# Optimization experiments

Measured on AMD Instinct MI355X. Metric: run time of the kernel, lower is better.

Reference implementation:

```python
import jax, jax.numpy as jnp
import numpy as np

NH = 16          # num_attention_heads
SMAX = 400.0     # smax for previous-task gates

def _gelu(x):
    return jax.nn.gelu(x, approximate=False)

def setup_inputs() -> dict:
    key = jax.random.key(0)
    ks = jax.random.split(key, 18)
    B, S, H, A, N = 8, 2048, 1024, 512, 10
    sc = lambda fan: 1.0 / np.sqrt(fan)
    f32 = jnp.float32
    return {
        "x":     jax.random.normal(ks[0], (B, S, H), f32),
        "fc1_w": jax.random.normal(ks[1], (A, H), f32) * sc(H),
        "fc1_b": jnp.zeros((A,), f32),
        "fc2_w": jax.random.normal(ks[2], (H, A), f32) * sc(A),
        "fc2_b": jnp.zeros((H,), f32),
        "efc1":  jax.random.normal(ks[3], (N, A), f32),
        "efc2":  jax.random.normal(ks[4], (N, H), f32),
        "etask": jax.random.normal(ks[5], (N, H), f32),
        "q_w":   jax.random.normal(ks[6], (H, H), f32) * sc(H),
        "q_b":   jnp.zeros((H,), f32),
        "k_w":   jax.random.normal(ks[7], (H, H), f32) * sc(H),
        "k_b":   jnp.zeros((H,), f32),
        "v_w":   jax.random.normal(ks[8], (H, H), f32) * sc(H),
        "v_b":   jnp.zeros((H,), f32),
        "equery": jax.random.normal(ks[9],  (N, H), f32),
        "ekey":   jax.random.normal(ks[10], (N, H), f32),
        "evalue": jax.random.normal(ks[11], (N, H), f32),
        "t": 5,
        "s": 400,
    }

def reference(x, fc1_w, fc1_b, fc2_w, fc2_b, efc1, efc2, etask,
              q_w, q_b, k_w, k_b, v_w, v_b, equery, ekey, evalue, t, s):
    B, S, H = x.shape
    hd = H // NH
    s = jnp.float32(s)

    # --- current-task gated adapter: h = act(fc2(act(fc1(x)) * gfc1)) * gfc2 ---
    h1 = _gelu(x @ fc1_w.T + fc1_b)                         # [B,S,A]
    gfc1 = jax.nn.sigmoid(s * efc1[t])                      # [A]
    gfc2 = jax.nn.sigmoid(s * efc2[t])                      # [H]
    h = _gelu((h1 * gfc1) @ fc2_w.T + fc2_b) * gfc2         # [B,S,H]

    # --- previous tasks (detached, gates at smax); vectorized over pre_t ---
    pg1 = jax.nn.sigmoid(SMAX * efc1[:t])                   # [t,A]
    pg2 = jax.nn.sigmoid(SMAX * efc2[:t])                   # [t,H]
    pre_h1 = h1[:, None, :, :] * pg1[None, :, None, :]      # [B,t,S,A]
    pre_h = _gelu(jnp.einsum('btsa,ha->btsh', pre_h1, fc2_w) + fc2_b)
    pre_h = jax.lax.stop_gradient(pre_h * pg2[None, :, None, :])  # [B,t,S,H]

    hid = jnp.concatenate([h[:, None], pre_h], axis=1)      # [B,T,S,H], T=t+1
    Tn = t + 1

    # --- task-gated QKV ---
    t_emb = jnp.broadcast_to(etask[t], (B, 1, S, H))        # query_states
    gq = jax.nn.sigmoid(s * equery[t])
    gk = jax.nn.sigmoid(s * ekey[t])
    gv = jax.nn.sigmoid(s * evalue[t])
    q = (t_emb @ q_w.T + q_b) * gq                          # [B,1,S,H]
    k = (hid @ k_w.T + k_b) * gk                            # [B,T,S,H]
    v = (hid @ v_w.T + v_b) * gv                            # [B,T,S,H]

    q5 = q.reshape(B, 1, S, NH, hd)
    k5 = k.reshape(B, Tn, S, NH, hd)
    v5 = v.reshape(B, Tn, S, NH, hd)

    # torch permute algebra: contract over heads (n), softmax over tasks (t)
    scores = jnp.einsum('bqsnd,btsnd->bdsqt', q5, k5) / np.sqrt(hd)  # [B,hd,S,1,T]
    probs = jax.nn.softmax(scores, axis=-1)
    ctx = jnp.einsum('bdsqt,btsnd->bdsqn', probs, v5)       # [B,hd,S,1,NH]
    ctx = ctx[:, :, :, 0, :].transpose(0, 2, 1, 3).reshape(B, S, H)

    return x + ctx
```

## Files before the change

kernel.cpp:

```cpp
#include <hip/hip_runtime.h>
#include <hip/hip_bf16.h>

static constexpr int B_ = 8, S_ = 2048, H_ = 1024, A_ = 512;
static constexpr int M_ = B_ * S_;
static constexpr int T_ = 6;
static constexpr long HID_STRIDE = (long)M_ * H_;
static constexpr long SC_STRIDE  = (long)M_ * 64;

typedef __attribute__((ext_vector_type(4))) float f32x4;
typedef __attribute__((ext_vector_type(8))) short bf16x8;

__device__ __forceinline__ float bf2f(ushort u){ return __uint_as_float(((unsigned)u) << 16); }
__device__ __forceinline__ ushort f2bf(float f){
  __hip_bfloat16 h = __float2bfloat16(f);
  return __builtin_bit_cast(unsigned short, h);
}
__device__ __forceinline__ float geluf(float x){
  return 0.5f * x * (1.0f + erff(x * 0.70710678118654752440f));
}
__device__ __forceinline__ float sigm(float x){ return 1.0f / (1.0f + __expf(-x)); }

__device__ __forceinline__ void gload_lds16(const void* g, void* l){
  __builtin_amdgcn_global_load_lds((const __attribute__((address_space(1))) void*)g,
                                   (__attribute__((address_space(3))) void*)l, 16, 0, 0);
}


__global__ void gates_kernel(const float* __restrict__ efc1, const float* __restrict__ efc2,
                             const int* __restrict__ tptr, const int* __restrict__ sptr,
                             float* __restrict__ g1, float* __restrict__ g2)
{
  const int h = threadIdx.x;
  const int t = *tptr;
  const float s = (float)(*sptr);
  #pragma unroll
  for (int ti = 0; ti < T_; ++ti) {
    const int task = (ti == 0) ? t : (ti - 1);
    const float scl = (ti == 0) ? s : 400.0f;
    g2[ti * H_ + h] = sigm(scl * efc2[task * H_ + h]);
    if (h < A_) g1[ti * A_ + h] = sigm(scl * efc1[task * A_ + h]);
  }
}

__global__ void kq_kernel(const float* __restrict__ etask, const float* __restrict__ q_w,
                          const float* __restrict__ q_b, const float* __restrict__ equery,
                          const float* __restrict__ ekey, const float* __restrict__ k_w,
                          const float* __restrict__ k_b,
                          const int* __restrict__ tptr, const int* __restrict__ sptr,
                          ushort* __restrict__ kqw, float* __restrict__ kqb)
{
  __shared__ float qg[16];
  const int d = blockIdx.x;
  const int tid = threadIdx.x;
  const int t = *tptr;
  const float s = (float)(*sptr);
  if (tid < 16) {
    const int hp = tid * 64 + d;
    const float* et = etask + (long)t * H_;
    const float* qw = q_w + (long)hp * H_;
    float acc = 0.f;
    for (int i = 0; i < H_; ++i) acc += et[i] * qw[i];
    float qv = (acc + q_b[hp]) * sigm(s * equery[t * H_ + hp]);
    qg[tid] = qv * sigm(s * ekey[t * H_ + hp]);
  }
  __syncthreads();
  for (int hh = tid; hh < H_; hh += 256) {
    float acc = 0.f;
    #pragma unroll
    for (int n = 0; n < 16; ++n) acc += qg[n] * k_w[(long)(n * 64 + d) * H_ + hh];
    kqw[d * H_ + hh] = f2bf(acc);
  }
  if (tid == 0) {
    float acc = 0.f;
    #pragma unroll
    for (int n = 0; n < 16; ++n) acc += qg[n] * k_b[n * 64 + d];
    kqb[d] = acc;
  }
}

__global__ void conv_bf16(const float* __restrict__ in, ushort* __restrict__ outp, long n)
{
  long i = ((long)blockIdx.x * blockDim.x + threadIdx.x) * 4;
  const long stride = (long)gridDim.x * blockDim.x * 4;
  for (; i < n; i += stride) {
    float4 v = *(const float4*)(in + i);
    ushort4 o;
    o.x = f2bf(v.x); o.y = f2bf(v.y); o.z = f2bf(v.z); o.w = f2bf(v.w);
    *(ushort4*)(outp + i) = o;
  }
}

__global__ void conv_w2g(const float* __restrict__ fc2w, const float* __restrict__ g1,
                         ushort* __restrict__ W2g)
{
  const long total = (long)T_ * H_ * A_;
  long i = ((long)blockIdx.x * blockDim.x + threadIdx.x) * 4;
  if (i >= total) return;
  const int ti = (int)(i / ((long)H_ * A_));
  const long r = i - (long)ti * H_ * A_;
  const int a = (int)(r & (A_ - 1));
  float4 wv = *(const float4*)(fc2w + r);
  const float* g = g1 + ti * A_ + a;
  ushort4 o;
  o.x = f2bf(wv.x * g[0]); o.y = f2bf(wv.y * g[1]);
  o.z = f2bf(wv.z * g[2]); o.w = f2bf(wv.w * g[3]);
  *(ushort4*)(W2g + i) = o;
}

__global__ void conv_vw(const float* __restrict__ v_w, const float* __restrict__ v_b,
                        const float* __restrict__ evalue,
                        const int* __restrict__ tptr, const int* __restrict__ sptr,
                        ushort* __restrict__ vwb, float* __restrict__ vbg)
{
  const int t = *tptr;
  const float s = (float)(*sptr);
  long i = ((long)blockIdx.x * blockDim.x + threadIdx.x) * 4;
  if (i < (long)H_ * H_) {
    const int f = (int)(i >> 10);
    const int hp = ((f & 15) << 6) + (f >> 4);
    const float g = sigm(s * evalue[t * H_ + hp]);
    float4 wv = *(const float4*)(v_w + ((long)hp << 10) + (i & 1023));
    ushort4 o;
    o.x = f2bf(wv.x * g); o.y = f2bf(wv.y * g);
    o.z = f2bf(wv.z * g); o.w = f2bf(wv.w * g);
    *(ushort4*)(vwb + i) = o;
  }
  const long j = (long)blockIdx.x * blockDim.x + threadIdx.x;
  if (j < H_) {
    const int hp = (((int)j & 15) << 6) + ((int)j >> 4);
    vbg[j] = v_b[hp] * sigm(s * evalue[t * H_ + hp]);
  }
}

template<int BM, int BN, int EPI>
__global__ __launch_bounds__(256)
void gemm_bt(const ushort* __restrict__ A, const ushort* __restrict__ Bm,
             void* __restrict__ C, const float* __restrict__ bias,
             const float* __restrict__ scale,
             int M, int N, int K,
             long strideAz, long strideBz, long strideCz, int strideSz,
             float postmul)
{
  constexpr int BK = 32;
  constexpr int WM = BM / 2, WN = BN / 2;
  constexpr int MI = WM / 16, NI = WN / 16;
  constexpr int L = BM / 64 + BN / 64;
  __shared__ alignas(16) ushort As[2][BM * BK];
  __shared__ alignas(16) ushort Bs[2][BN * BK];

  const int z = blockIdx.z;
  A  += (long)z * strideAz;
  Bm += (long)z * strideBz;

  const int gx = gridDim.x, gy = gridDim.y;
  int flat = blockIdx.y * gx + blockIdx.x;
  const int nwg = gx * gy;
  if ((nwg & 7) == 0) flat = (flat & 7) * (nwg >> 3) + (flat >> 3);
  const int m0 = (flat / gy) * BM, n0 = (flat % gy) * BN;

  const int tid = threadIdx.x, lane = tid & 63, wid = tid >> 6;
  const int wr = wid >> 1, wc = wid & 1;
  const int srow = tid >> 2;
  const int scol = (tid & 3) * 8;
  const int scol_src = (((tid & 3) ^ ((tid >> 3) & 3))) * 8;

  auto stage = [&](int buf, int kk) {
    #pragma unroll
    for (int i = 0; i < BM / 64; ++i)
      gload_lds16(A + (long)(m0 + i * 64 + srow) * K + kk + scol_src,
                  &As[buf][(i * 64 + srow) * BK + scol]);
    #pragma unroll
    for (int i = 0; i < BN / 64; ++i)
      gload_lds16(Bm + (long)(n0 + i * 64 + srow) * K + kk + scol_src,
                  &Bs[buf][(i * 64 + srow) * BK + scol]);
  };

  f32x4 acc[MI][NI] = {};
  const int NT = K / BK;
  const int ks = (((lane >> 4) ^ ((lane >> 1) & 3))) * 8;

  stage(0, 0);
  stage(1, BK);

  int cur = 0;
  for (int t = 0; t < NT; ++t) {
    if (t + 1 < NT) {
      if constexpr (L == 4) asm volatile("s_waitcnt vmcnt(4)" ::: "memory");
      else                  asm volatile("s_waitcnt vmcnt(3)" ::: "memory");
    } else {
      asm volatile("s_waitcnt vmcnt(0)" ::: "memory");
    }
    __builtin_amdgcn_s_barrier();
    __builtin_amdgcn_sched_barrier(0);

    bf16x8 af[MI], bfr[NI];
    #pragma unroll
    for (int m = 0; m < MI; ++m)
      af[m] = *(const bf16x8*)&As[cur][(wr * WM + m * 16 + (lane & 15)) * BK + ks];
    #pragma unroll
    for (int n = 0; n < NI; ++n)
      bfr[n] = *(const bf16x8*)&Bs[cur][(wc * WN + n * 16 + (lane & 15)) * BK + ks];
    asm volatile("s_waitcnt lgkmcnt(0)" ::: "memory");
    __builtin_amdgcn_sched_barrier(0);
    __builtin_amdgcn_s_barrier();
    __builtin_amdgcn_sched_barrier(0);

    if (t + 2 < NT) stage(cur, (t + 2) * BK);

    __builtin_amdgcn_s_setprio(1);
    #pragma unroll
    for (int m = 0; m < MI; ++m)
      #pragma unroll
      for (int n = 0; n < NI; ++n)
        acc[m][n] = __builtin_amdgcn_mfma_f32_16x16x32_bf16(af[m], bfr[n], acc[m][n], 0, 0, 0);
    __builtin_amdgcn_s_setprio(0);
    cur ^= 1;
  }

  const float* sc = (EPI == 1) ? (scale + (long)z * strideSz) : nullptr;
  #pragma unroll
  for (int m = 0; m < MI; ++m) {
    #pragma unroll
    for (int n = 0; n < NI; ++n) {
      const int col = n0 + wc * WN + n * 16 + (lane & 15);
      const float bv = bias[col];
      #pragma unroll
      for (int r = 0; r < 4; ++r) {
        const int row = m0 + wr * WM + m * 16 + (lane >> 4) * 4 + r;
        const float v = acc[m][n][r] + bv;
        const long ci = (long)z * strideCz + (long)row * N + col;
        if constexpr (EPI == 0) {
          ((ushort*)C)[ci] = f2bf(geluf(v));
        } else if constexpr (EPI == 1) {
          ((ushort*)C)[ci] = f2bf(geluf(v) * sc[col]);
        } else {
          ((float*)C)[ci] = v * postmul;
        }
      }
    }
  }
}

__global__ __launch_bounds__(256)
void fusedv_kernel(const ushort* __restrict__ hidb, const ushort* __restrict__ vwb,
                   const float* __restrict__ scB, const float* __restrict__ vbg,
                   const float* __restrict__ x, float* __restrict__ out)
{
  constexpr int BM = 128, BN = 128, BK = 32;
  constexpr int WM = 64, WN = 64, MI = 4, NI = 4;
  constexpr int NT = T_ * 32;
  __shared__ alignas(16) ushort As[2][BM * BK];
  __shared__ alignas(16) ushort Bs[2][BN * BK];
  __shared__ alignas(16) float p_lds[T_ * BM * 8];

  const int gx = gridDim.x, gy = gridDim.y;
  int flat = blockIdx.y * gx + blockIdx.x;
  const int nwg = gx * gy;
  flat = (flat & 7) * (nwg >> 3) + (flat >> 3);
  const int m0 = (flat / gy) * BM, n0 = (flat % gy) * BN;
  const int d0 = n0 >> 4;

  const int tid = threadIdx.x, lane = tid & 63, wid = tid >> 6;
  const int wr = wid >> 1, wc = wid & 1;
  const int srow = tid >> 2;
  const int scol = (tid & 3) * 8;
  const int scol_src = (((tid & 3) ^ ((tid >> 3) & 3))) * 8;
  const int ks = (((lane >> 4) ^ ((lane >> 1) & 3))) * 8;

  auto stageAB = [&](int buf, int kt) {
    const int ti = kt >> 5;
    const int kk = (kt & 31) << 5;
    const ushort* Ap = hidb + (long)ti * HID_STRIDE;
    #pragma unroll
    for (int i = 0; i < 2; ++i)
      gload_lds16(Ap + (long)(m0 + i * 64 + srow) * H_ + kk + scol_src,
                  &As[buf][(i * 64 + srow) * BK + scol]);
    #pragma unroll
    for (int i = 0; i < 2; ++i)
      gload_lds16(vwb + (long)(n0 + i * 64 + srow) * H_ + kk + scol_src,
                  &Bs[buf][(i * 64 + srow) * BK + scol]);
  };

  stageAB(0, 0);
  #pragma unroll
  for (int c = 0; c < 4; ++c) {
    const int cell = tid + c * 256;
    const int row = cell >> 3, dl = cell & 7;
    const long base = (long)(m0 + row) * 64 + d0 + dl;
    float v[T_]; float mx = -1e30f;
    #pragma unroll
    for (int ti = 0; ti < T_; ++ti) {
      v[ti] = scB[(long)ti * SC_STRIDE + base];
      mx = fmaxf(mx, v[ti]);
    }
    float sum = 0.f;
    #pragma unroll
    for (int ti = 0; ti < T_; ++ti) { v[ti] = __expf(v[ti] - mx); sum += v[ti]; }
    const float inv = 1.0f / sum;
    #pragma unroll
    for (int ti = 0; ti < T_; ++ti) p_lds[(ti * BM + row) * 8 + dl] = v[ti] * inv;
  }
  asm volatile("s_waitcnt lgkmcnt(0)" ::: "memory");
  stageAB(1, 1);

  const f32x4 zero = {};
  f32x4 ctx[MI][NI] = {};
  f32x4 acc[MI][NI] = {};

  int cur = 0;
  for (int kt = 0; kt < NT; ++kt) {
    if (kt + 1 < NT) asm volatile("s_waitcnt vmcnt(4)" ::: "memory");
    else             asm volatile("s_waitcnt vmcnt(0)" ::: "memory");
    __builtin_amdgcn_s_barrier();
    __builtin_amdgcn_sched_barrier(0);

    bf16x8 af[MI], bfr[NI];
    #pragma unroll
    for (int m = 0; m < MI; ++m)
      af[m] = *(const bf16x8*)&As[cur][(wr * WM + m * 16 + (lane & 15)) * BK + ks];
    #pragma unroll
    for (int n = 0; n < NI; ++n)
      bfr[n] = *(const bf16x8*)&Bs[cur][(wc * WN + n * 16 + (lane & 15)) * BK + ks];
    asm volatile("s_waitcnt lgkmcnt(0)" ::: "memory");
    __builtin_amdgcn_sched_barrier(0);
    __builtin_amdgcn_s_barrier();
    __builtin_amdgcn_sched_barrier(0);

    if (kt + 2 < NT) stageAB(cur, kt + 2);

    __builtin_amdgcn_s_setprio(1);
    #pragma unroll
    for (int m = 0; m < MI; ++m)
      #pragma unroll
      for (int n = 0; n < NI; ++n)
        acc[m][n] = __builtin_amdgcn_mfma_f32_16x16x32_bf16(af[m], bfr[n], acc[m][n], 0, 0, 0);
    __builtin_amdgcn_s_setprio(0);

    if ((kt & 31) == 31) {
      const int ti = kt >> 5;
      #pragma unroll
      for (int m = 0; m < MI; ++m) {
        #pragma unroll
        for (int r = 0; r < 4; ++r) {
          const int rowl = wr * WM + m * 16 + (lane >> 4) * 4 + r;
          const f32x4 pv = *(const f32x4*)&p_lds[(ti * BM + rowl) * 8 + wc * 4];
          #pragma unroll
          for (int n = 0; n < NI; ++n)
            ctx[m][n][r] += pv[n] * acc[m][n][r];
        }
        #pragma unroll
        for (int n = 0; n < NI; ++n) acc[m][n] = zero;
      }
    }
    cur ^= 1;
  }

  #pragma unroll
  for (int m = 0; m < MI; ++m) {
    #pragma unroll
    for (int n = 0; n < NI; ++n) {
      const int col = n0 + wc * WN + n * 16 + (lane & 15);
      const float bv = vbg[col];
      #pragma unroll
      for (int r = 0; r < 4; ++r) {
        const int row = m0 + wr * WM + m * 16 + (lane >> 4) * 4 + r;
        const long ci = (long)row * H_ + col;
        out[ci] = x[ci] + ctx[m][n][r] + bv;
      }
    }
  }
}

extern "C" void kernel_launch(void* const* d_in, const int* in_sizes, int n_in,
                              void* d_out, int out_size, void* d_ws, size_t ws_size,
                              hipStream_t stream)
{
  const float* x      = (const float*)d_in[0];
  const float* fc1_w  = (const float*)d_in[1];
  const float* fc1_b  = (const float*)d_in[2];
  const float* fc2_w  = (const float*)d_in[3];
  const float* fc2_b  = (const float*)d_in[4];
  const float* efc1   = (const float*)d_in[5];
  const float* efc2   = (const float*)d_in[6];
  const float* etask  = (const float*)d_in[7];
  const float* q_w    = (const float*)d_in[8];
  const float* q_b    = (const float*)d_in[9];
  const float* k_w    = (const float*)d_in[10];
  const float* k_b    = (const float*)d_in[11];
  const float* v_w    = (const float*)d_in[12];
  const float* v_b    = (const float*)d_in[13];
  const float* equery = (const float*)d_in[14];
  const float* ekey   = (const float*)d_in[15];
  const float* evalue = (const float*)d_in[16];
  const int*   tptr   = (const int*)d_in[17];
  const int*   sptr   = (const int*)d_in[18];
  float* out = (float*)d_out;

  char* w = (char*)d_ws;
  ushort* hidb = (ushort*)w; w += (long)T_ * M_ * H_ * 2;
  char* regionA = w;         w += (long)M_ * H_ * 2;
  ushort* xb  = (ushort*)regionA;
  float*  scB = (float*)regionA;
  ushort* h1b  = (ushort*)w; w += (long)M_ * A_ * 2;
  ushort* w1b  = (ushort*)w; w += (long)A_ * H_ * 2;
  ushort* W2g  = (ushort*)w; w += (long)T_ * H_ * A_ * 2;
  ushort* vwb  = (ushort*)w; w += (long)H_ * H_ * 2;
  ushort* kqw  = (ushort*)w; w += (long)64 * H_ * 2;
  float*  kqb  = (float*)w;  w += 64 * 4;
  float*  g1   = (float*)w;  w += T_ * A_ * 4;
  float*  g2   = (float*)w;  w += T_ * H_ * 4;
  float*  vbg  = (float*)w;  w += H_ * 4;
  (void)ws_size; (void)in_sizes; (void)n_in; (void)out_size;

  gates_kernel<<<1, 1024, 0, stream>>>(efc1, efc2, tptr, sptr, g1, g2);
  kq_kernel<<<64, 256, 0, stream>>>(etask, q_w, q_b, equery, ekey, k_w, k_b,
                                    tptr, sptr, kqw, kqb);
  conv_vw<<<1024, 256, 0, stream>>>(v_w, v_b, evalue, tptr, sptr, vwb, vbg);

  conv_bf16<<<2048, 256, 0, stream>>>(x, xb, (long)M_ * H_);
  conv_bf16<<<256, 256, 0, stream>>>(fc1_w, w1b, (long)A_ * H_);
  conv_w2g<<<3072, 256, 0, stream>>>(fc2_w, g1, W2g);

  gemm_bt<128, 128, 0><<<dim3(M_ / 128, A_ / 128, 1), 256, 0, stream>>>(
      xb, w1b, h1b, fc1_b, nullptr, M_, A_, H_, 0, 0, 0, 0, 0.f);

  gemm_bt<128, 128, 1><<<dim3(M_ / 128, H_ / 128, T_), 256, 0, stream>>>(
      h1b, W2g, hidb, fc2_b, g2, M_, H_, A_,
      0, (long)H_ * A_, HID_STRIDE, H_, 0.f);

  gemm_bt<128, 64, 2><<<dim3(M_ / 128, 1, T_), 256, 0, stream>>>(
      hidb, kqw, scB, kqb, nullptr, M_, 64, H_,
      HID_STRIDE, 0, SC_STRIDE, 0, 0.125f);

  fusedv_kernel<<<dim3(M_ / 128, H_ / 128, 1), 256, 0, stream>>>(
      hidb, vwb, scB, vbg, x, out);
}
```

Measured before the change: 560.7 us.

## Deepen GEMM pipelines to four LDS stages with register double-buffered fragments

Measured after the change: 947.9 us. 69.1% more time.

```diff
diff --git a/kernel.cpp b/kernel.cpp
--- a/kernel.cpp
+++ b/kernel.cpp
@@ -9,6 +9,7 @@
 
 typedef __attribute__((ext_vector_type(4))) float f32x4;
 typedef __attribute__((ext_vector_type(8))) short bf16x8;
+typedef __attribute__((ext_vector_type(4))) _Float16 f16x4;
 
 __device__ __forceinline__ float bf2f(ushort u){ return __uint_as_float(((unsigned)u) << 16); }
 __device__ __forceinline__ ushort f2bf(float f){
@@ -145,8 +146,8 @@
   constexpr int WM = BM / 2, WN = BN / 2;
   constexpr int MI = WM / 16, NI = WN / 16;
   constexpr int L = BM / 64 + BN / 64;
-  __shared__ alignas(16) ushort As[2][BM * BK];
-  __shared__ alignas(16) ushort Bs[2][BN * BK];
+  __shared__ alignas(16) ushort As[4][BM * BK];
+  __shared__ alignas(16) ushort Bs[4][BN * BK];
 
   const int z = blockIdx.z;
   A  += (long)z * strideAz;
@@ -163,6 +164,7 @@
   const int srow = tid >> 2;
   const int scol = (tid & 3) * 8;
   const int scol_src = (((tid & 3) ^ ((tid >> 3) & 3))) * 8;
+  const int ks = (((lane >> 4) ^ ((lane >> 1) & 3))) * 8;
 
   auto stage = [&](int buf, int kk) {
     #pragma unroll
@@ -174,47 +176,59 @@
       gload_lds16(Bm + (long)(n0 + i * 64 + srow) * K + kk + scol_src,
                   &Bs[buf][(i * 64 + srow) * BK + scol]);
   };
+  auto readF = [&](int buf, bf16x8* af, bf16x8* bfr) {
+    #pragma unroll
+    for (int m = 0; m < MI; ++m)
+      af[m] = *(const bf16x8*)&As[buf][(wr * WM + m * 16 + (lane & 15)) * BK + ks];
+    #pragma unroll
+    for (int n = 0; n < NI; ++n)
+      bfr[n] = *(const bf16x8*)&Bs[buf][(wc * WN + n * 16 + (lane & 15)) * BK + ks];
+  };
 
   f32x4 acc[MI][NI] = {};
   const int NT = K / BK;
-  const int ks = (((lane >> 4) ^ ((lane >> 1) & 3))) * 8;
-
-  stage(0, 0);
-  stage(1, BK);
-
-  int cur = 0;
-  for (int t = 0; t < NT; ++t) {
-    if (t + 1 < NT) {
+
+  stage(0, 0); stage(1, BK); stage(2, 2 * BK);
+  if constexpr (L == 4) asm volatile("s_waitcnt vmcnt(8)" ::: "memory");
+  else                  asm volatile("s_waitcnt vmcnt(6)" ::: "memory");
+  __builtin_amdgcn_s_barrier();
+  __builtin_amdgcn_sched_barrier(0);
+
+  bf16x8 afA[MI], bfrA[NI], afB[MI], bfrB[NI];
+  readF(0, afA, bfrA);
+
+  for (int t = 0; t < NT; t += 2) {
+    if (t + 2 < NT) {
       if constexpr (L == 4) asm volatile("s_waitcnt vmcnt(4)" ::: "memory");
       else                  asm volatile("s_waitcnt vmcnt(3)" ::: "memory");
-    } else {
-      asm volatile("s_waitcnt vmcnt(0)" ::: "memory");
-    }
+    } else asm volatile("s_waitcnt vmcnt(0)" ::: "memory");
     __builtin_amdgcn_s_barrier();
     __builtin_amdgcn_sched_barrier(0);
-
-    bf16x8 af[MI], bfr[NI];
-    #pragma unroll
-    for (int m = 0; m < MI; ++m)
-      af[m] = *(const bf16x8*)&As[cur][(wr * WM + m * 16 + (lane & 15)) * BK + ks];
-    #pragma unroll
-    for (int n = 0; n < NI; ++n)
-      bfr[n] = *(const bf16x8*)&Bs[cur][(wc * WN + n * 16 + (lane & 15)) * BK + ks];
-    asm volatile("s_waitcnt lgkmcnt(0)" ::: "memory");
-    __builtin_amdgcn_sched_barrier(0);
+    if (t + 3 < NT) stage((t + 3) & 3, (t + 3) * BK);
+    readF((t + 1) & 3, afB, bfrB);
+    __builtin_amdgcn_s_setprio(1);
+    #pragma unroll
+    for (int m = 0; m < MI; ++m)
+      #pragma unroll
+      for (int n = 0; n < NI; ++n)
+        acc[m][n] = __builtin_amdgcn_mfma_f32_16x16x32_bf16(afA[m], bfrA[n], acc[m][n], 0, 0, 0);
+    __builtin_amdgcn_s_setprio(0);
+
+    if (t + 3 < NT) {
+      if constexpr (L == 4) asm volatile("s_waitcnt vmcnt(4)" ::: "memory");
+      else                  asm volatile("s_waitcnt vmcnt(3)" ::: "memory");
+    } else asm volatile("s_waitcnt vmcnt(0)" ::: "memory");
     __builtin_amdgcn_s_barrier();
     __builtin_amdgcn_sched_barrier(0);
-
-    if (t + 2 < NT) stage(cur, (t + 2) * BK);
-
+    if (t + 4 < NT) stage((t + 4) & 3, (t + 4) * BK);
+    if (t + 2 < NT) readF((t + 2) & 3, afA, bfrA);
     __builtin_amdgcn_s_setprio(1);
     #pragma unroll
     for (int m = 0; m < MI; ++m)
       #pragma unroll
       for (int n = 0; n < NI; ++n)
-        acc[m][n] = __builtin_amdgcn_mfma_f32_16x16x32_bf16(af[m], bfr[n], acc[m][n], 0, 0, 0);
+        acc[m][n] = __builtin_amdgcn_mfma_f32_16x16x32_bf16(afB[m], bfrB[n], acc[m][n], 0, 0, 0);
     __builtin_amdgcn_s_setprio(0);
-    cur ^= 1;
   }
 
   const float* sc = (EPI == 1) ? (scale + (long)z * strideSz) : nullptr;
@@ -249,9 +263,9 @@
   constexpr int BM = 128, BN = 128, BK = 32;
   constexpr int WM = 64, WN = 64, MI = 4, NI = 4;
   constexpr int NT = T_ * 32;
-  __shared__ alignas(16) ushort As[2][BM * BK];
-  __shared__ alignas(16) ushort Bs[2][BN * BK];
-  __shared__ alignas(16) float p_lds[T_ * BM * 8];
+  __shared__ alignas(16) ushort As[4][BM * BK];
+  __shared__ alignas(16) ushort Bs[4][BN * BK];
+  __shared__ alignas(16) _Float16 p_lds[T_ * BM * 8];
 
   const int gx = gridDim.x, gy = gridDim.y;
   int flat = blockIdx.y * gx + blockIdx.x;
@@ -279,6 +293,14 @@
     for (int i = 0; i < 2; ++i)
       gload_lds16(vwb + (long)(n0 + i * 64 + srow) * H_ + kk + scol_src,
                   &Bs[buf][(i * 64 + srow) * BK + scol]);
+  };
+  auto readF = [&](int buf, bf16x8* af, bf16x8* bfr) {
+    #pragma unroll
+    for (int m = 0; m < MI; ++m)
+      af[m] = *(const bf16x8*)&As[buf][(wr * WM + m * 16 + (lane & 15)) * BK + ks];
+    #pragma unroll
+    for (int n = 0; n < NI; ++n)
+      bfr[n] = *(const bf16x8*)&Bs[buf][(wc * WN + n * 16 + (lane & 15)) * BK + ks];
   };
 
   stageAB(0, 0);
@@ -298,61 +320,66 @@
     for (int ti = 0; ti < T_; ++ti) { v[ti] = __expf(v[ti] - mx); sum += v[ti]; }
     const float inv = 1.0f / sum;
     #pragma unroll
-    for (int ti = 0; ti < T_; ++ti) p_lds[(ti * BM + row) * 8 + dl] = v[ti] * inv;
+    for (int ti = 0; ti < T_; ++ti) p_lds[(ti * BM + row) * 8 + dl] = (_Float16)(v[ti] * inv);
   }
   asm volatile("s_waitcnt lgkmcnt(0)" ::: "memory");
-  stageAB(1, 1);
+  stageAB(1, 1); stageAB(2, 2);
+
+  asm volatile("s_waitcnt vmcnt(8)" ::: "memory");
+  __builtin_amdgcn_s_barrier();
+  __builtin_amdgcn_sched_barrier(0);
 
   const f32x4 zero = {};
   f32x4 ctx[MI][NI] = {};
   f32x4 acc[MI][NI] = {};
-
-  int cur = 0;
-  for (int kt = 0; kt < NT; ++kt) {
-    if (kt + 1 < NT) asm volatile("s_waitcnt vmcnt(4)" ::: "memory");
-    else             asm volatile("s_waitcnt vmcnt(0)" ::: "memory");
+  bf16x8 afA[MI], bfrA[NI], afB[MI], bfrB[NI];
+  readF(0, afA, bfrA);
+
+  for (int t = 0; t < NT; t += 2) {
+    if (t + 2 < NT) asm volatile("s_waitcnt vmcnt(4)" ::: "memory");
+    else            asm volatile("s_waitcnt vmcnt(0)" ::: "memory");
     __builtin_amdgcn_s_barrier();
     __builtin_amdgcn_sched_barrier(0);
-
-    bf16x8 af[MI], bfr[NI];
-    #pragma unroll
-    for (int m = 0; m < MI; ++m)
-      af[m] = *(const bf16x8*)&As[cur][(wr * WM + m * 16 + (lane & 15)) * BK + ks];
-    #pragma unroll
-    for (int n = 0; n < NI; ++n)
-      bfr[n] = *(const bf16x8*)&Bs[cur][(wc * WN + n * 16 + (lane & 15)) * BK + ks];
-    asm volatile("s_waitcnt lgkmcnt(0)" ::: "memory");
-    __builtin_amdgcn_sched_barrier(0);
+    if (t + 3 < NT) stageAB((t + 3) & 3, t + 3);
+    readF((t + 1) & 3, afB, bfrB);
+    __builtin_amdgcn_s_setprio(1);
+    #pragma unroll
+    for (int m = 0; m < MI; ++m)
+      #pragma unroll
+      for (int n = 0; n < NI; ++n)
+        acc[m][n] = __builtin_amdgcn_mfma_f32_16x16x32_bf16(afA[m], bfrA[n], acc[m][n], 0, 0, 0);
+    __builtin_amdgcn_s_setprio(0);
+
+    if (t + 3 < NT) asm volatile("s_waitcnt vmcnt(4)" ::: "memory");
+    else            asm volatile("s_waitcnt vmcnt(0)" ::: "memory");
     __builtin_amdgcn_s_barrier();
     __builtin_amdgcn_sched_barrier(0);
-
-    if (kt + 2 < NT) stageAB(cur, kt + 2);
-
+    if (t + 4 < NT) stageAB((t + 4) & 3, t + 4);
+    if (t + 2 < NT) readF((t + 2) & 3, afA, bfrA);
     __builtin_amdgcn_s_setprio(1);
     #pragma unroll
     for (int m = 0; m < MI; ++m)
       #pragma unroll
       for (int n = 0; n < NI; ++n)
-        acc[m][n] = __builtin_amdgcn_mfma_f32_16x16x32_bf16(af[m], bfr[n], acc[m][n], 0, 0, 0);
+        acc[m][n] = __builtin_amdgcn_mfma_f32_16x16x32_bf16(afB[m], bfrB[n], acc[m][n], 0, 0, 0);
     __builtin_amdgcn_s_setprio(0);
 
-    if ((kt & 31) == 31) {
-      const int ti = kt >> 5;
+    if (((t + 1) & 31) == 31) {
+      const int ti = (t + 1) >> 5;
       #pragma unroll
       for (int m = 0; m < MI; ++m) {
         #pragma unroll
         for (int r = 0; r < 4; ++r) {
           const int rowl = wr * WM + m * 16 + (lane >> 4) * 4 + r;
-          const f32x4 pv = *(const f32x4*)&p_lds[(ti * BM + rowl) * 8 + wc * 4];
+          const f16x4 ph = *(const f16x4*)&p_lds[(ti * BM + rowl) * 8 + wc * 4];
           #pragma unroll
           for (int n = 0; n < NI; ++n)
-            ctx[m][n][r] += pv[n] * acc[m][n][r];
+            ctx[m][n][r] += (float)ph[n] * acc[m][n][r];
         }
         #pragma unroll
         for (int n = 0; n < NI; ++n) acc[m][n] = zero;
       }
     }
-    cur ^= 1;
   }
 
   #pragma unroll
```
